# Optimization experiments

Measured on AMD Instinct MI355X. Metric: run time of the kernel, lower is better.

Reference implementation:

```python
import jax, jax.numpy as jnp
import numpy as np

B, H, S, D = 2, 16, 2048, 64
DROPOUT_RATE = 0.1
NEG = -1000000000.0


def setup_inputs() -> dict:
    k = jax.random.key(0)
    kq, kk, kv, km = jax.random.split(k, 4)
    return {
        "query": jax.random.normal(kq, (B, H, S, D), dtype=jnp.float32),
        "key": jax.random.normal(kk, (B, H, S, D), dtype=jnp.float32),
        "value": jax.random.normal(kv, (B, H, S, D), dtype=jnp.float32),
        "mask": jax.random.randint(km, (B, 1, 1, S), 0, 2, dtype=jnp.int32),
    }


def reference(query, key, value, mask):
    d_k = query.shape[-1]
    # scores: [B,H,S,S]
    scores = jnp.einsum("bhqd,bhkd->bhqk", query, key) / jnp.sqrt(
        jnp.asarray(d_k, query.dtype))
    scores = jnp.where(mask == 0, jnp.asarray(NEG, scores.dtype), scores)
    p_attn = jax.nn.softmax(scores, axis=-1)
    # dropout (train mode, inverted scaling) with a fixed key for determinism
    keep = jax.random.bernoulli(jax.random.key(42), 1.0 - DROPOUT_RATE,
                                p_attn.shape)
    p_attn = jnp.where(keep, p_attn / (1.0 - DROPOUT_RATE), 0.0).astype(
        p_attn.dtype)
    out = jnp.einsum("bhqk,bhkd->bhqd", p_attn, value)
    return (out, p_attn)
```

## Files before the change

kernel.cpp:

```cpp
#include <hip/hip_runtime.h>
#include <stdint.h>

#define H_N 16
#define S_N 2048
#define D_N 64
#define QB  64
#define KT  64

typedef __attribute__((ext_vector_type(8))) __bf16 bf16x8;
typedef __attribute__((ext_vector_type(4))) float f32x4;

__device__ __forceinline__ unsigned short f2bf(float f) {
  uint32_t u = __float_as_uint(f);
  u += 0x7FFFu + ((u >> 16) & 1u);
  return (unsigned short)(u >> 16);
}

__device__ __forceinline__ uint2 tf2x32(uint32_t c0, uint32_t c1) {
  const uint32_t K0 = 0u, K1 = 42u, K2 = 0x1BD11BDAu ^ 42u;
  uint32_t x0 = c0 + K0, x1 = c1 + K1;
#define TFR(r) x0 += x1; x1 = __builtin_rotateleft32(x1, r); x1 ^= x0;
  TFR(13) TFR(15) TFR(26) TFR(6)
  x0 += K1; x1 += K2 + 1u;
  TFR(17) TFR(29) TFR(16) TFR(24)
  x0 += K2; x1 += K0 + 2u;
  TFR(13) TFR(15) TFR(26) TFR(6)
  x0 += K0; x1 += K1 + 3u;
  TFR(17) TFR(29) TFR(16) TFR(24)
  x0 += K1; x1 += K2 + 4u;
  TFR(13) TFR(15) TFR(26) TFR(6)
  x0 += K2; x1 += K0 + 5u;
#undef TFR
  return make_uint2(x0, x1);
}

__device__ __forceinline__ bool keep_bit(uint32_t j) {
  uint2 o = tf2x32(0u, j);
  return (((o.x ^ o.y) >> 9) < 0x733333u);
}

__device__ __forceinline__ void stageTile(const float* __restrict__ g,
                                          unsigned short* __restrict__ lds, int tid) {
  const int row = tid >> 2;
  const int c4  = tid & 3;
  const float4* s = (const float4*)(g + (tid << 4));
  float4 a = s[0], b = s[1], c = s[2], d = s[3];
  uint4 q0, q1;
  q0.x = (uint32_t)f2bf(a.x) | ((uint32_t)f2bf(a.y) << 16);
  q0.y = (uint32_t)f2bf(a.z) | ((uint32_t)f2bf(a.w) << 16);
  q0.z = (uint32_t)f2bf(b.x) | ((uint32_t)f2bf(b.y) << 16);
  q0.w = (uint32_t)f2bf(b.z) | ((uint32_t)f2bf(b.w) << 16);
  q1.x = (uint32_t)f2bf(c.x) | ((uint32_t)f2bf(c.y) << 16);
  q1.y = (uint32_t)f2bf(c.z) | ((uint32_t)f2bf(c.w) << 16);
  q1.z = (uint32_t)f2bf(d.x) | ((uint32_t)f2bf(d.y) << 16);
  q1.w = (uint32_t)f2bf(d.z) | ((uint32_t)f2bf(d.w) << 16);
  const int rs = row & 7;
  *(uint4*)&lds[row * 64 + (((c4 * 2)     ^ rs) << 3)] = q0;
  *(uint4*)&lds[row * 64 + (((c4 * 2 + 1) ^ rs) << 3)] = q1;
}

__device__ __forceinline__ void stageTileT(const float* __restrict__ g,
                                           unsigned short* __restrict__ lds, int tid) {
  const int key = tid >> 2;
  const int c4  = tid & 3;
  const float4* s = (const float4*)(g + (tid << 4));
  float4 v0 = s[0], v1 = s[1], v2 = s[2], v3 = s[3];
  const int kc = key >> 3, ke = key & 7;
#define WRT(e, val) { const int dd = c4 * 16 + (e); \
    lds[dd * 64 + (((kc ^ (dd & 7)) << 3) | ke)] = f2bf(val); }
  WRT(0,  v0.x) WRT(1,  v0.y) WRT(2,  v0.z) WRT(3,  v0.w)
  WRT(4,  v1.x) WRT(5,  v1.y) WRT(6,  v1.z) WRT(7,  v1.w)
  WRT(8,  v2.x) WRT(9,  v2.y) WRT(10, v2.z) WRT(11, v2.w)
  WRT(12, v3.x) WRT(13, v3.y) WRT(14, v3.z) WRT(15, v3.w)
#undef WRT
}

__global__ __launch_bounds__(256, 6)
void attn_fused(const float* __restrict__ Q, const float* __restrict__ K,
                const float* __restrict__ V, const int* __restrict__ mask,
                float* __restrict__ outO, float* __restrict__ outP) {
  __shared__ uint4 smemRaw[1536];
  unsigned short* const sbase = (unsigned short*)smemRaw;
  unsigned short* const sQ = sbase;
  unsigned short* const sK = sbase + 4096;
  unsigned short* const sV = sbase + 8192;
  unsigned short* const sP = sbase;

  const int tid = threadIdx.x;
  const int l   = tid & 63;
  const int w   = tid >> 6;
  const int bid = blockIdx.x;
  const int b   = bid & 1;
  const int h   = (bid >> 1) & (H_N - 1);
  const int qt  = bid >> 5;
  const int qBase = qt * QB;

  const int lrow = l & 15;
  const int lq4  = l >> 4;

  const size_t base = ((size_t)b * H_N + h) * (size_t)(S_N * D_N);
  const int* const maskRow = mask + b * S_N;

  stageTile(Q + base + (size_t)qBase * D_N, sQ, tid);
  __syncthreads();

  bf16x8 qf[2];
  {
    const int qrow = w * 16 + lrow;
#pragma unroll
    for (int ks = 0; ks < 2; ++ks) {
      const int cc = ks * 4 + lq4;
      qf[ks] = *(const bf16x8*)&sQ[qrow * 64 + ((cc ^ (qrow & 7)) << 3)];
    }
  }

  float minv[4];
  {
    float lsum[4] = {0.f, 0.f, 0.f, 0.f};
    for (int kt = 0; kt < S_N / KT; ++kt) {
      __syncthreads();
      stageTile(K + base + (size_t)(kt * KT) * D_N, sK, tid);
      __syncthreads();
#pragma unroll
      for (int n = 0; n < 4; ++n) {
        const int krow = n * 16 + lrow;
        f32x4 acc = {0.f, 0.f, 0.f, 0.f};
#pragma unroll
        for (int ks = 0; ks < 2; ++ks) {
          const int cc = ks * 4 + lq4;
          bf16x8 kf = *(const bf16x8*)&sK[krow * 64 + ((cc ^ (krow & 7)) << 3)];
          acc = __builtin_amdgcn_mfma_f32_16x16x32_bf16(qf[ks], kf, acc, 0, 0, 0);
        }
        const float mf = (float)maskRow[kt * KT + krow];
#pragma unroll
        for (int r = 0; r < 4; ++r)
          lsum[r] += mf * __expf(acc[r] * 0.125f - 20.0f);
      }
    }
#pragma unroll
    for (int r = 0; r < 4; ++r) {
      float v = lsum[r];
      v += __shfl_xor(v, 1);
      v += __shfl_xor(v, 2);
      v += __shfl_xor(v, 4);
      v += __shfl_xor(v, 8);
      minv[r] = (v > 0.f) ? ((1.0f / 0.9f) / v) : 0.f;
    }
  }

  f32x4 oacc[4];
#pragma unroll
  for (int n = 0; n < 4; ++n)
    oacc[n] = (f32x4){0.f, 0.f, 0.f, 0.f};

  const uint32_t qg = (uint32_t)(qBase + w * 16 + lq4 * 4);
  const size_t pBase = ((size_t)b * H_N + h) * (size_t)(S_N * S_N);
  const uint32_t jBase = (uint32_t)(b * H_N + h) * 4194304u + qg * 2048u;

  for (int kt = 0; kt < S_N / KT; ++kt) {
    __syncthreads();
    stageTile (K + base + (size_t)(kt * KT) * D_N, sK, tid);
    stageTileT(V + base + (size_t)(kt * KT) * D_N, sV, tid);
    __syncthreads();

#pragma unroll
    for (int n = 0; n < 4; ++n) {
      const int krow = n * 16 + lrow;
      f32x4 acc = {0.f, 0.f, 0.f, 0.f};
#pragma unroll
      for (int ks = 0; ks < 2; ++ks) {
        const int cc = ks * 4 + lq4;
        bf16x8 kf = *(const bf16x8*)&sK[krow * 64 + ((cc ^ (krow & 7)) << 3)];
        acc = __builtin_amdgcn_mfma_f32_16x16x32_bf16(qf[ks], kf, acc, 0, 0, 0);
      }
      const int kg = kt * KT + krow;
      const float mf = (float)maskRow[kg];
      const uint32_t j0 = jBase + (uint32_t)kg;
#pragma unroll
      for (int r = 0; r < 4; ++r) {
        const float pe = mf * __expf(acc[r] * 0.125f - 20.0f) * minv[r];
        const bool keep = keep_bit(j0 + (uint32_t)r * 2048u);
        const float pd = keep ? pe : 0.0f;
        __builtin_nontemporal_store(pd, &outP[pBase + (size_t)(qg + r) * S_N + (size_t)kg]);
        const int prow = w * 16 + lq4 * 4 + r;
        sP[prow * 64 + ((((krow >> 3) ^ (prow & 7)) << 3) | (krow & 7))] = f2bf(pd);
      }
    }
#pragma unroll
    for (int ks = 0; ks < 2; ++ks) {
      const int cc = ks * 4 + lq4;
      const int prow = w * 16 + lrow;
      bf16x8 af = *(const bf16x8*)&sP[prow * 64 + ((cc ^ (prow & 7)) << 3)];
#pragma unroll
      for (int n = 0; n < 4; ++n) {
        const int vrow = n * 16 + lrow;
        bf16x8 vf = *(const bf16x8*)&sV[vrow * 64 + ((cc ^ (vrow & 7)) << 3)];
        oacc[n] = __builtin_amdgcn_mfma_f32_16x16x32_bf16(af, vf, oacc[n], 0, 0, 0);
      }
    }
  }

#pragma unroll
  for (int n = 0; n < 4; ++n)
#pragma unroll
    for (int r = 0; r < 4; ++r) {
      const size_t off = (((size_t)b * H_N + h) * S_N + (size_t)(qg + r)) * D_N + n * 16 + lrow;
      __builtin_nontemporal_store(oacc[n][r], &outO[off]);
    }
}

extern "C" void kernel_launch(void* const* d_in, const int* in_sizes, int n_in,
                              void* d_out, int out_size, void* d_ws, size_t ws_size,
                              hipStream_t stream) {
  const float* Q   = (const float*)d_in[0];
  const float* K   = (const float*)d_in[1];
  const float* V   = (const float*)d_in[2];
  const int* mask  = (const int*)d_in[3];
  float* outO = (float*)d_out;
  float* outP = outO + (size_t)2 * H_N * S_N * D_N;
  hipLaunchKernelGGL(attn_fused, dim3(1024), dim3(256), 0, stream,
                     Q, K, V, mask, outO, outP);
}
```

Baseline: 436.4 us.

## Split key tile across two wave groups and prefetch K/V tiles into registers

Doubles the block to 512 threads so that two groups of four waves each handle half of every 64-key tile, with row sums combined through a small shared array. Global loads for the next K/V tile are issued into registers before compute on the current tile, to overlap memory latency. The keep test is rewritten to compare the full 32-bit hash directly instead of shifting it first. This adds an extra barrier per tile and raises register pressure under the new launch bounds.

```diff
diff --git a/kernel.cpp b/kernel.cpp
--- a/kernel.cpp
+++ b/kernel.cpp
@@ -36,59 +36,57 @@
 
 __device__ __forceinline__ bool keep_bit(uint32_t j) {
   uint2 o = tf2x32(0u, j);
-  return (((o.x ^ o.y) >> 9) < 0x733333u);
-}
-
-__device__ __forceinline__ void stageTile(const float* __restrict__ g,
-                                          unsigned short* __restrict__ lds, int tid) {
-  const int row = tid >> 2;
-  const int c4  = tid & 3;
-  const float4* s = (const float4*)(g + (tid << 4));
-  float4 a = s[0], b = s[1], c = s[2], d = s[3];
-  uint4 q0, q1;
-  q0.x = (uint32_t)f2bf(a.x) | ((uint32_t)f2bf(a.y) << 16);
-  q0.y = (uint32_t)f2bf(a.z) | ((uint32_t)f2bf(a.w) << 16);
-  q0.z = (uint32_t)f2bf(b.x) | ((uint32_t)f2bf(b.y) << 16);
-  q0.w = (uint32_t)f2bf(b.z) | ((uint32_t)f2bf(b.w) << 16);
-  q1.x = (uint32_t)f2bf(c.x) | ((uint32_t)f2bf(c.y) << 16);
-  q1.y = (uint32_t)f2bf(c.z) | ((uint32_t)f2bf(c.w) << 16);
-  q1.z = (uint32_t)f2bf(d.x) | ((uint32_t)f2bf(d.y) << 16);
-  q1.w = (uint32_t)f2bf(d.z) | ((uint32_t)f2bf(d.w) << 16);
-  const int rs = row & 7;
-  *(uint4*)&lds[row * 64 + (((c4 * 2)     ^ rs) << 3)] = q0;
-  *(uint4*)&lds[row * 64 + (((c4 * 2 + 1) ^ rs) << 3)] = q1;
-}
-
-__device__ __forceinline__ void stageTileT(const float* __restrict__ g,
-                                           unsigned short* __restrict__ lds, int tid) {
-  const int key = tid >> 2;
-  const int c4  = tid & 3;
-  const float4* s = (const float4*)(g + (tid << 4));
-  float4 v0 = s[0], v1 = s[1], v2 = s[2], v3 = s[3];
+  return ((o.x ^ o.y) < 0xE6666600u);
+}
+
+struct StageReg8 { float4 a, b; };
+
+__device__ __forceinline__ void stageLoad8(const float* __restrict__ g, int tid,
+                                           StageReg8& r) {
+  const float4* s = (const float4*)(g + (tid << 3));
+  r.a = s[0]; r.b = s[1];
+}
+
+__device__ __forceinline__ void stageWrite8(const StageReg8& r,
+                                            unsigned short* __restrict__ lds, int tid) {
+  const int row = tid >> 3;
+  const int c   = tid & 7;
+  uint4 q;
+  q.x = (uint32_t)f2bf(r.a.x) | ((uint32_t)f2bf(r.a.y) << 16);
+  q.y = (uint32_t)f2bf(r.a.z) | ((uint32_t)f2bf(r.a.w) << 16);
+  q.z = (uint32_t)f2bf(r.b.x) | ((uint32_t)f2bf(r.b.y) << 16);
+  q.w = (uint32_t)f2bf(r.b.z) | ((uint32_t)f2bf(r.b.w) << 16);
+  *(uint4*)&lds[row * 64 + ((c ^ (row & 7)) << 3)] = q;
+}
+
+__device__ __forceinline__ void stageWriteT8(const StageReg8& r,
+                                             unsigned short* __restrict__ lds, int tid) {
+  const int key = tid >> 3;
+  const int d0  = (tid & 7) * 8;
   const int kc = key >> 3, ke = key & 7;
-#define WRT(e, val) { const int dd = c4 * 16 + (e); \
+#define WRT(e, val) { const int dd = d0 + (e); \
     lds[dd * 64 + (((kc ^ (dd & 7)) << 3) | ke)] = f2bf(val); }
-  WRT(0,  v0.x) WRT(1,  v0.y) WRT(2,  v0.z) WRT(3,  v0.w)
-  WRT(4,  v1.x) WRT(5,  v1.y) WRT(6,  v1.z) WRT(7,  v1.w)
-  WRT(8,  v2.x) WRT(9,  v2.y) WRT(10, v2.z) WRT(11, v2.w)
-  WRT(12, v3.x) WRT(13, v3.y) WRT(14, v3.z) WRT(15, v3.w)
+  WRT(0, r.a.x) WRT(1, r.a.y) WRT(2, r.a.z) WRT(3, r.a.w)
+  WRT(4, r.b.x) WRT(5, r.b.y) WRT(6, r.b.z) WRT(7, r.b.w)
 #undef WRT
 }
 
-__global__ __launch_bounds__(256, 6)
+__global__ __launch_bounds__(512, 8)
 void attn_fused(const float* __restrict__ Q, const float* __restrict__ K,
                 const float* __restrict__ V, const int* __restrict__ mask,
                 float* __restrict__ outO, float* __restrict__ outP) {
   __shared__ uint4 smemRaw[1536];
+  __shared__ float part[2][64];
   unsigned short* const sbase = (unsigned short*)smemRaw;
-  unsigned short* const sQ = sbase;
-  unsigned short* const sK = sbase + 4096;
-  unsigned short* const sV = sbase + 8192;
-  unsigned short* const sP = sbase;
+  unsigned short* const sQP = sbase;
+  unsigned short* const sK  = sbase + 4096;
+  unsigned short* const sV  = sbase + 8192;
 
   const int tid = threadIdx.x;
   const int l   = tid & 63;
   const int w   = tid >> 6;
+  const int wq  = w & 3;
+  const int wk  = w >> 2;
   const int bid = blockIdx.x;
   const int b   = bid & 1;
   const int h   = (bid >> 1) & (H_N - 1);
@@ -101,29 +99,37 @@
   const size_t base = ((size_t)b * H_N + h) * (size_t)(S_N * D_N);
   const int* const maskRow = mask + b * S_N;
 
-  stageTile(Q + base + (size_t)qBase * D_N, sQ, tid);
+  {
+    StageReg8 qreg;
+    stageLoad8(Q + base + (size_t)qBase * D_N, tid, qreg);
+    stageWrite8(qreg, sQP, tid);
+  }
   __syncthreads();
 
   bf16x8 qf[2];
   {
-    const int qrow = w * 16 + lrow;
+    const int qrow = wq * 16 + lrow;
 #pragma unroll
     for (int ks = 0; ks < 2; ++ks) {
       const int cc = ks * 4 + lq4;
-      qf[ks] = *(const bf16x8*)&sQ[qrow * 64 + ((cc ^ (qrow & 7)) << 3)];
+      qf[ks] = *(const bf16x8*)&sQP[qrow * 64 + ((cc ^ (qrow & 7)) << 3)];
     }
   }
 
   float minv[4];
   {
     float lsum[4] = {0.f, 0.f, 0.f, 0.f};
+    StageReg8 kreg;
+    stageLoad8(K + base, tid, kreg);
     for (int kt = 0; kt < S_N / KT; ++kt) {
       __syncthreads();
-      stageTile(K + base + (size_t)(kt * KT) * D_N, sK, tid);
-      __syncthreads();
-#pragma unroll
-      for (int n = 0; n < 4; ++n) {
-        const int krow = n * 16 + lrow;
+      stageWrite8(kreg, sK, tid);
+      __syncthreads();
+      if (kt + 1 < S_N / KT)
+        stageLoad8(K + base + (size_t)((kt + 1) * KT) * D_N, tid, kreg);
+#pragma unroll
+      for (int n = 0; n < 2; ++n) {
+        const int krow = wk * 32 + n * 16 + lrow;
         f32x4 acc = {0.f, 0.f, 0.f, 0.f};
 #pragma unroll
         for (int ks = 0; ks < 2; ++ks) {
@@ -144,67 +150,83 @@
       v += __shfl_xor(v, 2);
       v += __shfl_xor(v, 4);
       v += __shfl_xor(v, 8);
+      if (lrow == 0) part[wk][wq * 16 + lq4 * 4 + r] = v;
+    }
+    __syncthreads();
+#pragma unroll
+    for (int r = 0; r < 4; ++r) {
+      const int row = wq * 16 + lq4 * 4 + r;
+      const float v = part[0][row] + part[1][row];
       minv[r] = (v > 0.f) ? ((1.0f / 0.9f) / v) : 0.f;
     }
   }
 
-  f32x4 oacc[4];
-#pragma unroll
-  for (int n = 0; n < 4; ++n)
-    oacc[n] = (f32x4){0.f, 0.f, 0.f, 0.f};
-
-  const uint32_t qg = (uint32_t)(qBase + w * 16 + lq4 * 4);
+  f32x4 oacc[2];
+  oacc[0] = (f32x4){0.f, 0.f, 0.f, 0.f};
+  oacc[1] = (f32x4){0.f, 0.f, 0.f, 0.f};
+
+  const uint32_t qg = (uint32_t)(qBase + wq * 16 + lq4 * 4);
   const size_t pBase = ((size_t)b * H_N + h) * (size_t)(S_N * S_N);
   const uint32_t jBase = (uint32_t)(b * H_N + h) * 4194304u + qg * 2048u;
 
-  for (int kt = 0; kt < S_N / KT; ++kt) {
-    __syncthreads();
-    stageTile (K + base + (size_t)(kt * KT) * D_N, sK, tid);
-    stageTileT(V + base + (size_t)(kt * KT) * D_N, sV, tid);
-    __syncthreads();
-
-#pragma unroll
-    for (int n = 0; n < 4; ++n) {
-      const int krow = n * 16 + lrow;
-      f32x4 acc = {0.f, 0.f, 0.f, 0.f};
+  {
+    StageReg8 kreg, vreg;
+    stageLoad8(K + base, tid, kreg);
+    stageLoad8(V + base, tid, vreg);
+    for (int kt = 0; kt < S_N / KT; ++kt) {
+      __syncthreads();
+      stageWrite8 (kreg, sK, tid);
+      stageWriteT8(vreg, sV, tid);
+      __syncthreads();
+      if (kt + 1 < S_N / KT) {
+        stageLoad8(K + base + (size_t)((kt + 1) * KT) * D_N, tid, kreg);
+        stageLoad8(V + base + (size_t)((kt + 1) * KT) * D_N, tid, vreg);
+      }
+
+#pragma unroll
+      for (int n = 0; n < 2; ++n) {
+        const int krow = wk * 32 + n * 16 + lrow;
+        f32x4 acc = {0.f, 0.f, 0.f, 0.f};
+#pragma unroll
+        for (int ks = 0; ks < 2; ++ks) {
+          const int cc = ks * 4 + lq4;
+          bf16x8 kf = *(const bf16x8*)&sK[krow * 64 + ((cc ^ (krow & 7)) << 3)];
+          acc = __builtin_amdgcn_mfma_f32_16x16x32_bf16(qf[ks], kf, acc, 0, 0, 0);
+        }
+        const int kg = kt * KT + krow;
+        const float mf = (float)maskRow[kg];
+        const uint32_t j0 = jBase + (uint32_t)kg;
+#pragma unroll
+        for (int r = 0; r < 4; ++r) {
+          const float pe = mf * __expf(acc[r] * 0.125f - 20.0f) * minv[r];
+          const float pd = keep_bit(j0 + (uint32_t)r * 2048u) ? pe : 0.0f;
+          __builtin_nontemporal_store(pd, &outP[pBase + (size_t)(qg + r) * S_N + (size_t)kg]);
+          const int prow = wq * 16 + lq4 * 4 + r;
+          sQP[prow * 64 + ((((krow >> 3) ^ (prow & 7)) << 3) | (krow & 7))] = f2bf(pd);
+        }
+      }
+      __syncthreads();
 #pragma unroll
       for (int ks = 0; ks < 2; ++ks) {
         const int cc = ks * 4 + lq4;
-        bf16x8 kf = *(const bf16x8*)&sK[krow * 64 + ((cc ^ (krow & 7)) << 3)];
-        acc = __builtin_amdgcn_mfma_f32_16x16x32_bf16(qf[ks], kf, acc, 0, 0, 0);
-      }
-      const int kg = kt * KT + krow;
-      const float mf = (float)maskRow[kg];
-      const uint32_t j0 = jBase + (uint32_t)kg;
-#pragma unroll
-      for (int r = 0; r < 4; ++r) {
-        const float pe = mf * __expf(acc[r] * 0.125f - 20.0f) * minv[r];
-        const bool keep = keep_bit(j0 + (uint32_t)r * 2048u);
-        const float pd = keep ? pe : 0.0f;
-        __builtin_nontemporal_store(pd, &outP[pBase + (size_t)(qg + r) * S_N + (size_t)kg]);
-        const int prow = w * 16 + lq4 * 4 + r;
-        sP[prow * 64 + ((((krow >> 3) ^ (prow & 7)) << 3) | (krow & 7))] = f2bf(pd);
-      }
-    }
-#pragma unroll
-    for (int ks = 0; ks < 2; ++ks) {
-      const int cc = ks * 4 + lq4;
-      const int prow = w * 16 + lrow;
-      bf16x8 af = *(const bf16x8*)&sP[prow * 64 + ((cc ^ (prow & 7)) << 3)];
-#pragma unroll
-      for (int n = 0; n < 4; ++n) {
-        const int vrow = n * 16 + lrow;
-        bf16x8 vf = *(const bf16x8*)&sV[vrow * 64 + ((cc ^ (vrow & 7)) << 3)];
-        oacc[n] = __builtin_amdgcn_mfma_f32_16x16x32_bf16(af, vf, oacc[n], 0, 0, 0);
-      }
-    }
-  }
-
-#pragma unroll
-  for (int n = 0; n < 4; ++n)
+        const int prow = wq * 16 + lrow;
+        bf16x8 af = *(const bf16x8*)&sQP[prow * 64 + ((cc ^ (prow & 7)) << 3)];
+#pragma unroll
+        for (int n = 0; n < 2; ++n) {
+          const int vrow = wk * 32 + n * 16 + lrow;
+          bf16x8 vf = *(const bf16x8*)&sV[vrow * 64 + ((cc ^ (vrow & 7)) << 3)];
+          oacc[n] = __builtin_amdgcn_mfma_f32_16x16x32_bf16(af, vf, oacc[n], 0, 0, 0);
+        }
+      }
+    }
+  }
+
+#pragma unroll
+  for (int n = 0; n < 2; ++n)
 #pragma unroll
     for (int r = 0; r < 4; ++r) {
-      const size_t off = (((size_t)b * H_N + h) * S_N + (size_t)(qg + r)) * D_N + n * 16 + lrow;
+      const size_t off = (((size_t)b * H_N + h) * S_N + (size_t)(qg + r)) * D_N
+                       + wk * 32 + n * 16 + lrow;
       __builtin_nontemporal_store(oacc[n][r], &outO[off]);
     }
 }
@@ -218,6 +240,6 @@
   const int* mask  = (const int*)d_in[3];
   float* outO = (float*)d_out;
   float* outP = outO + (size_t)2 * H_N * S_N * D_N;
-  hipLaunchKernelGGL(attn_fused, dim3(1024), dim3(256), 0, stream,
+  hipLaunchKernelGGL(attn_fused, dim3(1024), dim3(512), 0, stream,
                      Q, K, V, mask, outO, outP);
 }
```

Measured after the change: 533.3 us. 22.2% more time.
